# Kernel tuning notes

Hardware: AMD Instinct MI355X
Metric: run time of the kernel (lower is better)

## Reference

```python
import jax, jax.numpy as jnp
import numpy as np

C = 32  # channel dim ('size' in the torch module)


def setup_inputs() -> dict:
    key = jax.random.key(0)
    ks = jax.random.split(key, 9)
    B, H, W = 8, 64, 512
    shape = (B, C, H, W)
    q = jax.random.normal(ks[0], shape, dtype=jnp.float32)
    k = jax.random.normal(ks[1], shape, dtype=jnp.float32)
    v = jax.random.normal(ks[2], shape, dtype=jnp.float32)
    s = 1.0 / np.sqrt(C)  # kaiming-uniform-ish scale for 1x1 conv
    wq = jax.random.uniform(ks[3], (C, C), jnp.float32, -s, s)
    bq = jax.random.uniform(ks[4], (C,), jnp.float32, -s, s)
    wk = jax.random.uniform(ks[5], (C, C), jnp.float32, -s, s)
    bk = jax.random.uniform(ks[6], (C,), jnp.float32, -s, s)
    wv = jax.random.uniform(ks[7], (C, C), jnp.float32, -s, s)
    bv = jax.random.uniform(ks[8], (C,), jnp.float32, -s, s)
    return {"q": q, "k": k, "v": v, "wq": wq, "bq": bq,
            "wk": wk, "bk": bk, "wv": wv, "bv": bv}


def _proj(x, w, b):
    # 1x1 conv on NCHW == per-pixel linear over channels; emit NHWC directly
    return jnp.einsum('oc,bchw->bhwo', w, x) + b


def reference(q, k, v, wq, bq, wk, bk, wv, bv):
    residual = q  # [B,C,H,W]
    qp = _proj(q, wq, bq)  # [B,H,W,C]
    kp = _proj(k, wk, bk)
    vp = _proj(v, wv, bv)
    # unnormalized attention over the W axis, batched over (B,H)
    attn = jnp.einsum('bhwc,bhxc->bhwx', qp, kp)        # [B,H,W,W]
    att = jnp.einsum('bhwx,bhxc->bhwc', attn, vp)       # [B,H,W,C]
    out = jnp.transpose(att, (0, 3, 1, 2)) + residual   # back to NCHW
    return out
```

## Files before the change

### kernel.cpp

```cpp
#include <hip/hip_runtime.h>
#include <hip/hip_bf16.h>

#define CH   32
#define WD   512
#define NH   64
#define CHST (NH * WD)
#define BST  (CH * CHST)
#define ROWB 1040

typedef short bf16x8 __attribute__((ext_vector_type(8)));
typedef float f32x16 __attribute__((ext_vector_type(16)));

__device__ __forceinline__ unsigned short f2bf(float f) {
  union { __hip_bfloat16 h; unsigned short u; } cv;
  cv.h = __float2bfloat16(f);
  return cv.u;
}
__device__ __forceinline__ unsigned int pk2(float lo_, float hi_) {
  return ((unsigned int)f2bf(hi_) << 16) | (unsigned int)f2bf(lo_);
}
__device__ __forceinline__ void swap32(unsigned int& a, unsigned int& b) {
  asm volatile("v_permlane32_swap_b32 %0, %1" : "+v"(a), "+v"(b));
}

union W4 { unsigned int u[4]; bf16x8 v; };

__global__ __launch_bounds__(512, 4)
void fused_mha(const float* __restrict__ qg, const float* __restrict__ kg,
               const float* __restrict__ vg,
               const float* __restrict__ wqg, const float* __restrict__ bqg,
               const float* __restrict__ wkg, const float* __restrict__ bkg,
               const float* __restrict__ wvg, const float* __restrict__ bvg,
               float* __restrict__ outg)
{
  __shared__ __align__(16) char kpL[CH * ROWB];
  __shared__ __align__(16) char vpL[CH * ROWB];

  const int t = threadIdx.x, lane = t & 63, wid = t >> 6;
  const int lo = lane & 31, hi = lane >> 5;
  const int bh = blockIdx.x;
  const size_t base = (size_t)(bh >> 6) * BST + (size_t)(bh & 63) * WD;

  int rowr[16];
  #pragma unroll
  for (int r = 0; r < 16; ++r) rowr[r] = (r & 3) + 8 * (r >> 2) + 4 * hi;

  bf16x8 wkA[2], wvA[2];
  {
    const float* wk_r = wkg + lo * CH + 8 * hi;
    const float* wv_r = wvg + lo * CH + 8 * hi;
    #pragma unroll
    for (int s = 0; s < 2; ++s)
      #pragma unroll
      for (int j = 0; j < 8; ++j) {
        wkA[s][j] = (short)f2bf(wk_r[16 * s + j]);
        wvA[s][j] = (short)f2bf(wv_r[16 * s + j]);
      }
  }
  float bkr[16], bvr[16];
  #pragma unroll
  for (int r = 0; r < 16; ++r) { bkr[r] = bkg[rowr[r]]; bvr[r] = bvg[rowr[r]]; }

  #pragma unroll
  for (int it = 0; it < 2; ++it) {
    const int x0 = 64 * wid + 32 * it;
    float kf[16], vf[16];
    #pragma unroll
    for (int s = 0; s < 2; ++s)
      #pragma unroll
      for (int j = 0; j < 8; ++j) {
        kf[8 * s + j] = kg[base + (size_t)(16 * s + 8 * hi + j) * CHST + x0 + lo];
        vf[8 * s + j] = vg[base + (size_t)(16 * s + 8 * hi + j) * CHST + x0 + lo];
      }
    bf16x8 kb[2], vb[2];
    #pragma unroll
    for (int s = 0; s < 2; ++s)
      #pragma unroll
      for (int j = 0; j < 8; ++j) {
        kb[s][j] = (short)f2bf(kf[8 * s + j]);
        vb[s][j] = (short)f2bf(vf[8 * s + j]);
      }
    f32x16 ka, va;
    #pragma unroll
    for (int r = 0; r < 16; ++r) { ka[r] = bkr[r]; va[r] = bvr[r]; }
    ka = __builtin_amdgcn_mfma_f32_32x32x16_bf16(wkA[0], kb[0], ka, 0, 0, 0);
    ka = __builtin_amdgcn_mfma_f32_32x32x16_bf16(wkA[1], kb[1], ka, 0, 0, 0);
    va = __builtin_amdgcn_mfma_f32_32x32x16_bf16(wvA[0], vb[0], va, 0, 0, 0);
    va = __builtin_amdgcn_mfma_f32_32x32x16_bf16(wvA[1], vb[1], va, 0, 0, 0);
    #pragma unroll
    for (int r = 0; r < 16; ++r) {
      const int row = rowr[r];
      const int off = row * ROWB + ((((x0 + lo) << 1)) ^ (((row >> 3) & 3) << 4));
      *(unsigned short*)(kpL + off) = f2bf(ka[r]);
      *(unsigned short*)(vpL + off) = f2bf(va[r]);
    }
  }

  bf16x8 wqA[2];
  {
    float wqf[16];
    #pragma unroll
    for (int s = 0; s < 2; ++s)
      #pragma unroll
      for (int j = 0; j < 8; ++j)
        wqf[8 * s + j] = wqg[(16 * s + 8 * hi + j) * CH + lo];
    #pragma unroll
    for (int s = 0; s < 2; ++s)
      #pragma unroll
      for (int j = 0; j < 8; ++j)
        wqA[s][j] = (short)f2bf(wqf[8 * s + j]);
  }

  __syncthreads();

  float qpf[32];
  #pragma unroll
  for (int it = 0; it < 2; ++it)
    #pragma unroll
    for (int s = 0; s < 2; ++s)
      #pragma unroll
      for (int j = 0; j < 8; ++j)
        qpf[16 * it + 8 * s + j] =
            qg[base + (size_t)(16 * s + 8 * hi + j) * CHST + 64 * wid + 32 * it + lo];

  const int swzlo = ((lo >> 3) & 3) << 4;
  f32x16 macc;
  #pragma unroll
  for (int r = 0; r < 16; ++r) macc[r] = 0.f;
  #pragma unroll
  for (int kk = 0; kk < 32; ++kk) {
    const int off = lo * ROWB + ((32 * kk + 16 * hi) ^ swzlo);
    bf16x8 afr = *(const bf16x8*)(kpL + off);
    bf16x8 bfr = *(const bf16x8*)(vpL + off);
    macc = __builtin_amdgcn_mfma_f32_32x32x16_bf16(afr, bfr, macc, 0, 0, 0);
  }

  float bqr[16];
  #pragma unroll
  for (int r = 0; r < 16; ++r) bqr[r] = bqg[rowr[r]];

  W4 mb0, mb1;
  mb0.u[0] = pk2(macc[0], macc[1]);  mb0.u[1] = pk2(macc[2],  macc[3]);
  mb0.u[2] = pk2(macc[4], macc[5]);  mb0.u[3] = pk2(macc[6],  macc[7]);
  swap32(mb0.u[0], mb0.u[2]);        swap32(mb0.u[1], mb0.u[3]);
  mb1.u[0] = pk2(macc[8], macc[9]);  mb1.u[1] = pk2(macc[10], macc[11]);
  mb1.u[2] = pk2(macc[12], macc[13]); mb1.u[3] = pk2(macc[14], macc[15]);
  swap32(mb1.u[0], mb1.u[2]);        swap32(mb1.u[1], mb1.u[3]);

  f32x16 gacc;
  #pragma unroll
  for (int r = 0; r < 16; ++r) gacc[r] = 0.f;
  gacc = __builtin_amdgcn_mfma_f32_32x32x16_bf16(wqA[0], mb0.v, gacc, 0, 0, 0);
  gacc = __builtin_amdgcn_mfma_f32_32x32x16_bf16(wqA[1], mb1.v, gacc, 0, 0, 0);
  #pragma unroll
  for (int r = 0; r < 16; ++r)
    if (rowr[r] == lo) gacc[r] += 1.f;

  float part = 0.f;
  #pragma unroll
  for (int r = 0; r < 16; ++r) part = fmaf(bqr[r], macc[r], part);
  unsigned int pa = __float_as_uint(part), pb = pa;
  swap32(pa, pb);
  const float gv = __uint_as_float(pa) + __uint_as_float(pb);

  W4 ga0, ga1;
  ga0.u[0] = pk2(gacc[0], gacc[1]);   ga0.u[1] = pk2(gacc[2],  gacc[3]);
  ga0.u[2] = pk2(gacc[4], gacc[5]);   ga0.u[3] = pk2(gacc[6],  gacc[7]);
  swap32(ga0.u[0], ga0.u[2]);         swap32(ga0.u[1], ga0.u[3]);
  ga1.u[0] = pk2(gacc[8], gacc[9]);   ga1.u[1] = pk2(gacc[10], gacc[11]);
  ga1.u[2] = pk2(gacc[12], gacc[13]); ga1.u[3] = pk2(gacc[14], gacc[15]);
  swap32(ga1.u[0], ga1.u[2]);         swap32(ga1.u[1], ga1.u[3]);

  float gsh[16];
  #pragma unroll
  for (int r = 0; r < 16; ++r) gsh[r] = __shfl(gv, rowr[r], 64);

  #pragma unroll
  for (int it = 0; it < 2; ++it) {
    const int x0 = 64 * wid + 32 * it;
    bf16x8 qb[2];
    #pragma unroll
    for (int s = 0; s < 2; ++s)
      #pragma unroll
      for (int j = 0; j < 8; ++j)
        qb[s][j] = (short)f2bf(qpf[16 * it + 8 * s + j]);
    f32x16 acc;
    #pragma unroll
    for (int r = 0; r < 16; ++r) acc[r] = gsh[r];
    acc = __builtin_amdgcn_mfma_f32_32x32x16_bf16(ga0.v, qb[0], acc, 0, 0, 0);
    acc = __builtin_amdgcn_mfma_f32_32x32x16_bf16(ga1.v, qb[1], acc, 0, 0, 0);
    #pragma unroll
    for (int r = 0; r < 16; ++r)
      outg[base + (size_t)rowr[r] * CHST + x0 + lo] = acc[r];
  }
}

extern "C" void kernel_launch(void* const* d_in, const int* in_sizes, int n_in,
                              void* d_out, int out_size, void* d_ws, size_t ws_size,
                              hipStream_t stream) {
  const float* q  = (const float*)d_in[0];
  const float* k  = (const float*)d_in[1];
  const float* v  = (const float*)d_in[2];
  const float* wq = (const float*)d_in[3];
  const float* bq = (const float*)d_in[4];
  const float* wk = (const float*)d_in[5];
  const float* bk = (const float*)d_in[6];
  const float* wv = (const float*)d_in[7];
  const float* bv = (const float*)d_in[8];
  float* out = (float*)d_out;

  (void)in_sizes; (void)n_in; (void)out_size; (void)d_ws; (void)ws_size;

  fused_mha<<<dim3(8 * 64), dim3(512), 0, stream>>>(q, k, v, wq, bq, wk, bk, wv, bv, out);
}
```

Before: 31.64 us.

## Split fused attention kernel into reduction kernel and output kernel via workspace

The single fused kernel is split into two launches. The first computes the per-(b,h) 32x32 matrix G and the bias vector from k and v and writes them to workspace. The second reads q and G and writes the output using 1024 smaller blocks. The goal is to drop the q load and the output stage from the reduction kernel, easing register pressure, and to raise parallelism in the output phase. The cost is an extra kernel launch and a small global round-trip through the workspace.

Result: slower. 35.63 us (+12.6%).

```diff
diff --git a/kernel.cpp b/kernel.cpp
--- a/kernel.cpp
+++ b/kernel.cpp
@@ -26,12 +26,11 @@
 union W4 { unsigned int u[4]; bf16x8 v; };
 
 __global__ __launch_bounds__(512, 4)
-void fused_mha(const float* __restrict__ qg, const float* __restrict__ kg,
-               const float* __restrict__ vg,
-               const float* __restrict__ wqg, const float* __restrict__ bqg,
-               const float* __restrict__ wkg, const float* __restrict__ bkg,
-               const float* __restrict__ wvg, const float* __restrict__ bvg,
-               float* __restrict__ outg)
+void k1_Gg(const float* __restrict__ kg, const float* __restrict__ vg,
+           const float* __restrict__ wqg, const float* __restrict__ bqg,
+           const float* __restrict__ wkg, const float* __restrict__ bkg,
+           const float* __restrict__ wvg, const float* __restrict__ bvg,
+           unsigned short* __restrict__ GW, float* __restrict__ gw)
 {
   __shared__ __align__(16) char kpL[CH * ROWB];
   __shared__ __align__(16) char vpL[CH * ROWB];
@@ -113,16 +112,6 @@
 
   __syncthreads();
 
-  float qpf[32];
-  #pragma unroll
-  for (int it = 0; it < 2; ++it)
-    #pragma unroll
-    for (int s = 0; s < 2; ++s)
-      #pragma unroll
-      for (int j = 0; j < 8; ++j)
-        qpf[16 * it + 8 * s + j] =
-            qg[base + (size_t)(16 * s + 8 * hi + j) * CHST + 64 * wid + 32 * it + lo];
-
   const int swzlo = ((lo >> 3) & 3) << 4;
   f32x16 macc;
   #pragma unroll
@@ -140,12 +129,12 @@
   for (int r = 0; r < 16; ++r) bqr[r] = bqg[rowr[r]];
 
   W4 mb0, mb1;
-  mb0.u[0] = pk2(macc[0], macc[1]);  mb0.u[1] = pk2(macc[2],  macc[3]);
-  mb0.u[2] = pk2(macc[4], macc[5]);  mb0.u[3] = pk2(macc[6],  macc[7]);
-  swap32(mb0.u[0], mb0.u[2]);        swap32(mb0.u[1], mb0.u[3]);
-  mb1.u[0] = pk2(macc[8], macc[9]);  mb1.u[1] = pk2(macc[10], macc[11]);
+  mb0.u[0] = pk2(macc[0], macc[1]);   mb0.u[1] = pk2(macc[2],  macc[3]);
+  mb0.u[2] = pk2(macc[4], macc[5]);   mb0.u[3] = pk2(macc[6],  macc[7]);
+  swap32(mb0.u[0], mb0.u[2]);         swap32(mb0.u[1], mb0.u[3]);
+  mb1.u[0] = pk2(macc[8], macc[9]);   mb1.u[1] = pk2(macc[10], macc[11]);
   mb1.u[2] = pk2(macc[12], macc[13]); mb1.u[3] = pk2(macc[14], macc[15]);
-  swap32(mb1.u[0], mb1.u[2]);        swap32(mb1.u[1], mb1.u[3]);
+  swap32(mb1.u[0], mb1.u[2]);         swap32(mb1.u[1], mb1.u[3]);
 
   f32x16 gacc;
   #pragma unroll
@@ -171,13 +160,49 @@
   ga1.u[2] = pk2(gacc[12], gacc[13]); ga1.u[3] = pk2(gacc[14], gacc[15]);
   swap32(ga1.u[0], ga1.u[2]);         swap32(ga1.u[1], ga1.u[3]);
 
+  if (wid == 0) {
+    const int li = hi * 32 + lo;
+    *(bf16x8*)(GW + (size_t)bh * 1024 +       li * 8) = ga0.v;
+    *(bf16x8*)(GW + (size_t)bh * 1024 + 512 + li * 8) = ga1.v;
+    if (hi == 0) gw[bh * 32 + lo] = gv;
+  }
+}
+
+__global__ __launch_bounds__(256, 4)
+void k2_out(const float* __restrict__ qg, const unsigned short* __restrict__ GW,
+            const float* __restrict__ gw, float* __restrict__ outg)
+{
+  const int t = threadIdx.x, lane = t & 63, wid = t >> 6;
+  const int lo = lane & 31, hi = lane >> 5;
+  const int bid = blockIdx.x;
+  const int bh = bid >> 1, half = bid & 1;
+  const size_t base = (size_t)(bh >> 6) * BST + (size_t)(bh & 63) * WD;
+
+  int rowr[16];
+  #pragma unroll
+  for (int r = 0; r < 16; ++r) rowr[r] = (r & 3) + 8 * (r >> 2) + 4 * hi;
+
+  const int li = hi * 32 + lo;
+  bf16x8 ga0 = *(const bf16x8*)(GW + (size_t)bh * 1024 +       li * 8);
+  bf16x8 ga1 = *(const bf16x8*)(GW + (size_t)bh * 1024 + 512 + li * 8);
   float gsh[16];
   #pragma unroll
-  for (int r = 0; r < 16; ++r) gsh[r] = __shfl(gv, rowr[r], 64);
+  for (int r = 0; r < 16; ++r) gsh[r] = gw[bh * 32 + rowr[r]];
+
+  float qpf[32];
+  #pragma unroll
+  for (int it = 0; it < 2; ++it)
+    #pragma unroll
+    for (int s = 0; s < 2; ++s)
+      #pragma unroll
+      for (int j = 0; j < 8; ++j)
+        qpf[16 * it + 8 * s + j] =
+            qg[base + (size_t)(16 * s + 8 * hi + j) * CHST +
+               256 * half + 64 * wid + 32 * it + lo];
 
   #pragma unroll
   for (int it = 0; it < 2; ++it) {
-    const int x0 = 64 * wid + 32 * it;
+    const int x0 = 256 * half + 64 * wid + 32 * it;
     bf16x8 qb[2];
     #pragma unroll
     for (int s = 0; s < 2; ++s)
@@ -187,8 +212,8 @@
     f32x16 acc;
     #pragma unroll
     for (int r = 0; r < 16; ++r) acc[r] = gsh[r];
-    acc = __builtin_amdgcn_mfma_f32_32x32x16_bf16(ga0.v, qb[0], acc, 0, 0, 0);
-    acc = __builtin_amdgcn_mfma_f32_32x32x16_bf16(ga1.v, qb[1], acc, 0, 0, 0);
+    acc = __builtin_amdgcn_mfma_f32_32x32x16_bf16(ga0, qb[0], acc, 0, 0, 0);
+    acc = __builtin_amdgcn_mfma_f32_32x32x16_bf16(ga1, qb[1], acc, 0, 0, 0);
     #pragma unroll
     for (int r = 0; r < 16; ++r)
       outg[base + (size_t)rowr[r] * CHST + x0 + lo] = acc[r];
@@ -209,7 +234,11 @@
   const float* bv = (const float*)d_in[8];
   float* out = (float*)d_out;
 
-  (void)in_sizes; (void)n_in; (void)out_size; (void)d_ws; (void)ws_size;
-
-  fused_mha<<<dim3(8 * 64), dim3(512), 0, stream>>>(q, k, v, wq, bq, wk, bk, wv, bv, out);
-}
+  unsigned short* GW = (unsigned short*)d_ws;
+  float* gw = (float*)((char*)d_ws + 512 * 2048);
+
+  (void)in_sizes; (void)n_in; (void)out_size; (void)ws_size;
+
+  k1_Gg<<<dim3(512), dim3(512), 0, stream>>>(k, v, wq, bq, wk, bk, wv, bv, GW, gw);
+  k2_out<<<dim3(1024), dim3(256), 0, stream>>>(q, GW, gw, out);
+}
```

## Compute raw K^T V Gram matrix before projecting with Wk/Wv

Applied to the files above, without the earlier changes.

Instead of projecting K and V through their 1x1 convs per pixel and then forming Kp^T Vp, each block first forms the raw 32x32 K^T V product with MFMA from vectorized float loads, reduces it across waves in LDS, and applies Wk, Wv and the biases afterwards using channel sums. This removes the per-pixel projection MFMAs and the large bf16 K/V staging in LDS, replacing them with a small cross-wave reduction. Split hi/lo bf16 MFMAs are added to keep precision on the reassociated products. The risk is numerical drift from computing raw Gram sums in bf16.

After: 29.30 us. 7.4% less time.

```diff
diff --git a/kernel.cpp b/kernel.cpp
--- a/kernel.cpp
+++ b/kernel.cpp
@@ -6,24 +6,41 @@
 #define NH   64
 #define CHST (NH * WD)
 #define BST  (CH * CHST)
-#define ROWB 1040
+#define NST  36
 
 typedef short bf16x8 __attribute__((ext_vector_type(8)));
 typedef float f32x16 __attribute__((ext_vector_type(16)));
+typedef float f32x8  __attribute__((ext_vector_type(8)));
 
 __device__ __forceinline__ unsigned short f2bf(float f) {
   union { __hip_bfloat16 h; unsigned short u; } cv;
   cv.h = __float2bfloat16(f);
   return cv.u;
 }
+__device__ __forceinline__ float bf2f(unsigned short u) {
+  return __uint_as_float(((unsigned int)u) << 16);
+}
 __device__ __forceinline__ unsigned int pk2(float lo_, float hi_) {
   return ((unsigned int)f2bf(hi_) << 16) | (unsigned int)f2bf(lo_);
 }
 __device__ __forceinline__ void swap32(unsigned int& a, unsigned int& b) {
   asm volatile("v_permlane32_swap_b32 %0, %1" : "+v"(a), "+v"(b));
 }
-
 union W4 { unsigned int u[4]; bf16x8 v; };
+
+__device__ __forceinline__ void d2frag(const f32x16& d, W4& f0, W4& f1) {
+  f0.u[0] = pk2(d[0], d[1]);   f0.u[1] = pk2(d[2],  d[3]);
+  f0.u[2] = pk2(d[4], d[5]);   f0.u[3] = pk2(d[6],  d[7]);
+  swap32(f0.u[0], f0.u[2]);    swap32(f0.u[1], f0.u[3]);
+  f1.u[0] = pk2(d[8], d[9]);   f1.u[1] = pk2(d[10], d[11]);
+  f1.u[2] = pk2(d[12], d[13]); f1.u[3] = pk2(d[14], d[15]);
+  swap32(f1.u[0], f1.u[2]);    swap32(f1.u[1], f1.u[3]);
+}
+__device__ __forceinline__ float halfsum(float v) {
+  unsigned int a = __float_as_uint(v), b = a;
+  swap32(a, b);
+  return __uint_as_float(a) + __uint_as_float(b);
+}
 
 __global__ __launch_bounds__(512, 4)
 void fused_mha(const float* __restrict__ qg, const float* __restrict__ kg,
@@ -33,8 +50,8 @@
                const float* __restrict__ wvg, const float* __restrict__ bvg,
                float* __restrict__ outg)
 {
-  __shared__ __align__(16) char kpL[CH * ROWB];
-  __shared__ __align__(16) char vpL[CH * ROWB];
+  __shared__ float np[8][CH][NST];
+  __shared__ float sp[8][2][CH];
 
   const int t = threadIdx.x, lane = t & 63, wid = t >> 6;
   const int lo = lane & 31, hi = lane >> 5;
@@ -57,60 +74,56 @@
         wvA[s][j] = (short)f2bf(wv_r[16 * s + j]);
       }
   }
-  float bkr[16], bvr[16];
-  #pragma unroll
-  for (int r = 0; r < 16; ++r) { bkr[r] = bkg[rowr[r]]; bvr[r] = bvg[rowr[r]]; }
-
-  #pragma unroll
-  for (int it = 0; it < 2; ++it) {
-    const int x0 = 64 * wid + 32 * it;
-    float kf[16], vf[16];
-    #pragma unroll
-    for (int s = 0; s < 2; ++s)
-      #pragma unroll
-      for (int j = 0; j < 8; ++j) {
-        kf[8 * s + j] = kg[base + (size_t)(16 * s + 8 * hi + j) * CHST + x0 + lo];
-        vf[8 * s + j] = vg[base + (size_t)(16 * s + 8 * hi + j) * CHST + x0 + lo];
-      }
-    bf16x8 kb[2], vb[2];
-    #pragma unroll
-    for (int s = 0; s < 2; ++s)
-      #pragma unroll
-      for (int j = 0; j < 8; ++j) {
-        kb[s][j] = (short)f2bf(kf[8 * s + j]);
-        vb[s][j] = (short)f2bf(vf[8 * s + j]);
-      }
-    f32x16 ka, va;
-    #pragma unroll
-    for (int r = 0; r < 16; ++r) { ka[r] = bkr[r]; va[r] = bvr[r]; }
-    ka = __builtin_amdgcn_mfma_f32_32x32x16_bf16(wkA[0], kb[0], ka, 0, 0, 0);
-    ka = __builtin_amdgcn_mfma_f32_32x32x16_bf16(wkA[1], kb[1], ka, 0, 0, 0);
-    va = __builtin_amdgcn_mfma_f32_32x32x16_bf16(wvA[0], vb[0], va, 0, 0, 0);
-    va = __builtin_amdgcn_mfma_f32_32x32x16_bf16(wvA[1], vb[1], va, 0, 0, 0);
-    #pragma unroll
-    for (int r = 0; r < 16; ++r) {
-      const int row = rowr[r];
-      const int off = row * ROWB + ((((x0 + lo) << 1)) ^ (((row >> 3) & 3) << 4));
-      *(unsigned short*)(kpL + off) = f2bf(ka[r]);
-      *(unsigned short*)(vpL + off) = f2bf(va[r]);
-    }
-  }
-
-  bf16x8 wqA[2];
-  {
-    float wqf[16];
-    #pragma unroll
-    for (int s = 0; s < 2; ++s)
-      #pragma unroll
-      for (int j = 0; j < 8; ++j)
-        wqf[8 * s + j] = wqg[(16 * s + 8 * hi + j) * CH + lo];
-    #pragma unroll
-    for (int s = 0; s < 2; ++s)
-      #pragma unroll
-      for (int j = 0; j < 8; ++j)
-        wqA[s][j] = (short)f2bf(wqf[8 * s + j]);
-  }
-
+
+  const float* krow = kg + base + (size_t)lo * CHST + 64 * wid + 8 * hi;
+  const float* vrow = vg + base + (size_t)lo * CHST + 64 * wid + 8 * hi;
+  f32x8 kf[4], vf[4];
+  #pragma unroll
+  for (int kk = 0; kk < 4; ++kk) {
+    kf[kk] = *(const f32x8*)(krow + 16 * kk);
+    vf[kk] = *(const f32x8*)(vrow + 16 * kk);
+  }
+  f32x16 nacc;
+  #pragma unroll
+  for (int r = 0; r < 16; ++r) nacc[r] = 0.f;
+  float psK = 0.f, psV = 0.f;
+  #pragma unroll
+  for (int kk = 0; kk < 4; ++kk) {
+    W4 kb, vb;
+    #pragma unroll
+    for (int i = 0; i < 4; ++i) {
+      kb.u[i] = pk2(kf[kk][2 * i], kf[kk][2 * i + 1]);
+      vb.u[i] = pk2(vf[kk][2 * i], vf[kk][2 * i + 1]);
+    }
+    nacc = __builtin_amdgcn_mfma_f32_32x32x16_bf16(kb.v, vb.v, nacc, 0, 0, 0);
+    #pragma unroll
+    for (int j = 0; j < 8; ++j) { psK += kf[kk][j]; psV += vf[kk][j]; }
+  }
+  #pragma unroll
+  for (int r = 0; r < 16; ++r) np[wid][rowr[r]][lo] = nacc[r];
+  {
+    const float sk = halfsum(psK), sv = halfsum(psV);
+    if (hi == 0) { sp[wid][0][lo] = sk; sp[wid][1][lo] = sv; }
+  }
+  __syncthreads();
+
+  {
+    #pragma unroll
+    for (int p = 0; p < 2; ++p) {
+      const int e = t + 512 * p, o = e >> 5, c = e & 31;
+      float s = 0.f;
+      #pragma unroll
+      for (int w = 0; w < 8; ++w) s += np[w][o][c];
+      np[0][o][c] = s;
+    }
+    if (t < 64) {
+      const int j = t >> 5, o = t & 31;
+      float s = 0.f;
+      #pragma unroll
+      for (int w = 0; w < 8; ++w) s += sp[w][j][o];
+      sp[0][j][o] = s;
+    }
+  }
   __syncthreads();
 
   float qpf[32];
@@ -123,30 +136,63 @@
         qpf[16 * it + 8 * s + j] =
             qg[base + (size_t)(16 * s + 8 * hi + j) * CHST + 64 * wid + 32 * it + lo];
 
-  const int swzlo = ((lo >> 3) & 3) << 4;
-  f32x16 macc;
-  #pragma unroll
-  for (int r = 0; r < 16; ++r) macc[r] = 0.f;
-  #pragma unroll
-  for (int kk = 0; kk < 32; ++kk) {
-    const int off = lo * ROWB + ((32 * kk + 16 * hi) ^ swzlo);
-    bf16x8 afr = *(const bf16x8*)(kpL + off);
-    bf16x8 bfr = *(const bf16x8*)(vpL + off);
-    macc = __builtin_amdgcn_mfma_f32_32x32x16_bf16(afr, bfr, macc, 0, 0, 0);
-  }
-
-  float bqr[16];
-  #pragma unroll
-  for (int r = 0; r < 16; ++r) bqr[r] = bqg[rowr[r]];
-
+  bf16x8 wqA[2];
+  {
+    #pragma unroll
+    for (int s = 0; s < 2; ++s)
+      #pragma unroll
+      for (int j = 0; j < 8; ++j)
+        wqA[s][j] = (short)f2bf(wqg[(16 * s + 8 * hi + j) * CH + lo]);
+  }
+  float bkr[16], bqr[16];
+  #pragma unroll
+  for (int r = 0; r < 16; ++r) { bkr[r] = bkg[rowr[r]]; bqr[r] = bqg[rowr[r]]; }
+  const float bvlo = bvg[lo];
+
+  W4 NAh[2], NAl[2];
+  #pragma unroll
+  for (int s = 0; s < 2; ++s) {
+    f32x8 nf = *(const f32x8*)&np[0][lo][16 * s + 8 * hi];
+    #pragma unroll
+    for (int i = 0; i < 4; ++i) {
+      const float x = nf[2 * i], y = nf[2 * i + 1];
+      const unsigned short hx = f2bf(x), hy = f2bf(y);
+      NAh[s].u[i] = ((unsigned int)hy << 16) | hx;
+      NAl[s].u[i] = pk2(x - bf2f(hx), y - bf2f(hy));
+    }
+  }
+  f32x16 pacc;
+  #pragma unroll
+  for (int r = 0; r < 16; ++r) pacc[r] = 0.f;
+  pacc = __builtin_amdgcn_mfma_f32_32x32x16_bf16(NAh[0].v, wvA[0], pacc, 0, 0, 0);
+  pacc = __builtin_amdgcn_mfma_f32_32x32x16_bf16(NAh[1].v, wvA[1], pacc, 0, 0, 0);
+  pacc = __builtin_amdgcn_mfma_f32_32x32x16_bf16(NAl[0].v, wvA[0], pacc, 0, 0, 0);
+  pacc = __builtin_amdgcn_mfma_f32_32x32x16_bf16(NAl[1].v, wvA[1], pacc, 0, 0, 0);
+  f32x16 pp;
+  #pragma unroll
+  for (int r = 0; r < 16; ++r) pp[r] = pacc[r] + sp[0][0][rowr[r]] * bvlo;
+  float uprt = 0.f;
+  #pragma unroll
+  for (int s = 0; s < 2; ++s)
+    #pragma unroll
+    for (int j = 0; j < 8; ++j)
+      uprt += bf2f((unsigned short)wvA[s][j]) * sp[0][1][16 * s + 8 * hi + j];
+  const float uful = halfsum(uprt) + 512.f * bvlo;
+  f32x16 pres;
+  #pragma unroll
+  for (int r = 0; r < 16; ++r) pres[r] = pp[r] - bf2f(f2bf(pp[r]));
+  W4 pb0h, pb1h, pb0l, pb1l;
+  d2frag(pp, pb0h, pb1h);
+  d2frag(pres, pb0l, pb1l);
+  f32x16 mac;
+  #pragma unroll
+  for (int r = 0; r < 16; ++r) mac[r] = bkr[r] * uful;
+  mac = __builtin_amdgcn_mfma_f32_32x32x16_bf16(wkA[0], pb0h.v, mac, 0, 0, 0);
+  mac = __builtin_amdgcn_mfma_f32_32x32x16_bf16(wkA[1], pb1h.v, mac, 0, 0, 0);
+  mac = __builtin_amdgcn_mfma_f32_32x32x16_bf16(wkA[0], pb0l.v, mac, 0, 0, 0);
+  mac = __builtin_amdgcn_mfma_f32_32x32x16_bf16(wkA[1], pb1l.v, mac, 0, 0, 0);
   W4 mb0, mb1;
-  mb0.u[0] = pk2(macc[0], macc[1]);  mb0.u[1] = pk2(macc[2],  macc[3]);
-  mb0.u[2] = pk2(macc[4], macc[5]);  mb0.u[3] = pk2(macc[6],  macc[7]);
-  swap32(mb0.u[0], mb0.u[2]);        swap32(mb0.u[1], mb0.u[3]);
-  mb1.u[0] = pk2(macc[8], macc[9]);  mb1.u[1] = pk2(macc[10], macc[11]);
-  mb1.u[2] = pk2(macc[12], macc[13]); mb1.u[3] = pk2(macc[14], macc[15]);
-  swap32(mb1.u[0], mb1.u[2]);        swap32(mb1.u[1], mb1.u[3]);
-
+  d2frag(mac, mb0, mb1);
   f32x16 gacc;
   #pragma unroll
   for (int r = 0; r < 16; ++r) gacc[r] = 0.f;
@@ -155,22 +201,12 @@
   #pragma unroll
   for (int r = 0; r < 16; ++r)
     if (rowr[r] == lo) gacc[r] += 1.f;
-
   float part = 0.f;
   #pragma unroll
-  for (int r = 0; r < 16; ++r) part = fmaf(bqr[r], macc[r], part);
-  unsigned int pa = __float_as_uint(part), pb = pa;
-  swap32(pa, pb);
-  const float gv = __uint_as_float(pa) + __uint_as_float(pb);
-
+  for (int r = 0; r < 16; ++r) part = fmaf(bqr[r], mac[r], part);
+  const float gv = halfsum(part);
   W4 ga0, ga1;
-  ga0.u[0] = pk2(gacc[0], gacc[1]);   ga0.u[1] = pk2(gacc[2],  gacc[3]);
-  ga0.u[2] = pk2(gacc[4], gacc[5]);   ga0.u[3] = pk2(gacc[6],  gacc[7]);
-  swap32(ga0.u[0], ga0.u[2]);         swap32(ga0.u[1], ga0.u[3]);
-  ga1.u[0] = pk2(gacc[8], gacc[9]);   ga1.u[1] = pk2(gacc[10], gacc[11]);
-  ga1.u[2] = pk2(gacc[12], gacc[13]); ga1.u[3] = pk2(gacc[14], gacc[15]);
-  swap32(ga1.u[0], ga1.u[2]);         swap32(ga1.u[1], ga1.u[3]);
-
+  d2frag(gacc, ga0, ga1);
   float gsh[16];
   #pragma unroll
   for (int r = 0; r < 16; ++r) gsh[r] = __shfl(gv, rowr[r], 64);
```
